# Optimization experiments

Hardware: AMD Instinct MI355X
Metric: run time of the kernel (lower is better)

The kernel has to match this reference:

```python
import jax, jax.numpy as jnp
import numpy as np

B, S, H, K = 64, 512, 1024, 7

def setup_inputs() -> dict:
    key = jax.random.key(0)
    ks = jax.random.split(key, 7)
    x = jax.random.normal(ks[0], (B, S, H), dtype=jnp.float32)
    gt = jax.random.randint(ks[1], (B, S), 0, K, dtype=jnp.int64)
    mask = jnp.ones((B, S), dtype=bool)
    # learned parameters
    W = jax.random.normal(ks[2], (H, K), dtype=jnp.float32) * (1.0 / np.sqrt(H))
    b = jnp.zeros((K,), dtype=jnp.float32)
    start_trans = jax.random.uniform(ks[3], (K,), minval=-0.1, maxval=0.1)
    end_trans = jax.random.uniform(ks[4], (K,), minval=-0.1, maxval=0.1)
    trans = jax.random.uniform(ks[5], (K, K), minval=-0.1, maxval=0.1)
    return {"x": x, "gt": gt, "mask": mask, "W": W, "b": b,
            "start_trans": start_trans, "end_trans": end_trans, "trans": trans}

def _crf_neg_llh(emissions, gt, mask, start_trans, end_trans, trans):
    # emissions: [B,S,K], gt: [B,S] int, mask: [B,S] bool
    maskf = mask.astype(emissions.dtype)
    # ---- numerator: score of gold path ----
    em_at_tag = jnp.take_along_axis(emissions, gt[..., None], axis=-1)[..., 0]  # [B,S]
    trans_sc = trans[gt[:, :-1], gt[:, 1:]]                                      # [B,S-1]
    num = start_trans[gt[:, 0]] + em_at_tag[:, 0]
    num = num + jnp.sum((trans_sc + em_at_tag[:, 1:]) * maskf[:, 1:], axis=1)
    last_idx = jnp.sum(mask, axis=1).astype(jnp.int32) - 1                       # [B]
    last_tags = jnp.take_along_axis(gt, last_idx[:, None], axis=1)[:, 0]
    num = num + end_trans[last_tags]
    # ---- denominator: log partition via forward algorithm (lax.scan) ----
    alpha0 = start_trans[None, :] + emissions[:, 0]                              # [B,K]
    em_rest = jnp.transpose(emissions[:, 1:], (1, 0, 2))                         # [S-1,B,K]
    m_rest = jnp.transpose(mask[:, 1:], (1, 0))                                  # [S-1,B]
    def step(alpha, inp):
        em_t, m_t = inp
        nxt = jax.nn.logsumexp(alpha[:, :, None] + trans[None, :, :] + em_t[:, None, :], axis=1)
        return jnp.where(m_t[:, None], nxt, alpha), None
    alpha, _ = jax.lax.scan(step, alpha0, (em_rest, m_rest))
    denom = jax.nn.logsumexp(alpha + end_trans[None, :], axis=1)                 # [B]
    llh = num - denom
    return -jnp.mean(llh)  # reduction='mean', module returns negative

def reference(x, gt, mask, W, b, start_trans, end_trans, trans):
    emissions = jnp.einsum('bsh,hk->bsk', x, W) + b
    return _crf_neg_llh(emissions, gt, mask, start_trans, end_trans, trans)
```

## Files before the change

### kernel.cpp

```cpp
#include <hip/hip_runtime.h>
#include <math.h>

#define NB 64
#define NS 512
#define NH 1024
#define NK 7
#define NCHUNK 16
#define CLEN 32

#define WPACK_F4 (14 * 512)

__global__ __launch_bounds__(256) void pack_w(const float* __restrict__ W,
                                              float4* __restrict__ Wpack)
{
    const int idx = blockIdx.x * 256 + threadIdx.x;
    if (idx >= WPACK_F4) return;
    const int j    = idx >> 9;
    const int t    = idx & 511;
    const int lane = t & 63;
    const int half = (t >> 6) & 1;
    const int cc   = j / NK;
    const int k    = j - cc * NK;
    const int hbase = half * 512 + (cc * 64 + lane) * 4;
    float4 v;
    v.x = W[(hbase + 0) * NK + k];
    v.y = W[(hbase + 1) * NK + k];
    v.z = W[(hbase + 2) * NK + k];
    v.w = W[(hbase + 3) * NK + k];
    Wpack[idx] = v;
}

__global__ __launch_bounds__(512, 4) void fused_emis_chunk(
    const float* __restrict__ x, const float4* __restrict__ Wpack,
    const float* __restrict__ bias, const float* __restrict__ trans,
    float* __restrict__ em, float* __restrict__ chunkP)
{
    __shared__ float lds_half[CLEN][2][8];
    __shared__ float lds_em[CLEN * 8];
    __shared__ float lds_tr[49];

    const int tid  = threadIdx.x;
    const int lane = tid & 63;
    const int wave = tid >> 6;
    const int pair = wave >> 1;
    const int half = wave & 1;
    const int b = blockIdx.x >> 4;
    const int c = blockIdx.x & (NCHUNK - 1);
    const int t0 = c * CLEN;
    const int row0 = b * NS + t0;

    if (tid < 49) lds_tr[tid] = trans[tid];

    float4 w4[2][NK];
#pragma unroll
    for (int cc = 0; cc < 2; ++cc)
#pragma unroll
        for (int k = 0; k < NK; ++k)
            w4[cc][k] = Wpack[(cc * NK + k) * 512 + tid];

    const float4* xbase = (const float4*)(x + (size_t)row0 * NH) + half * 128 + lane;

#pragma unroll 2
    for (int s = 0; s < 8; ++s) {
        const int r = pair + 4 * s;
        const float4* xr = xbase + (size_t)r * (NH / 4);
        const float4 v0 = xr[0];
        const float4 v1 = xr[64];
        float acc[NK];
#pragma unroll
        for (int k = 0; k < NK; ++k)
            acc[k] = v0.x * w4[0][k].x + v0.y * w4[0][k].y
                   + v0.z * w4[0][k].z + v0.w * w4[0][k].w
                   + v1.x * w4[1][k].x + v1.y * w4[1][k].y
                   + v1.z * w4[1][k].z + v1.w * w4[1][k].w;
#pragma unroll
        for (int m = 1; m < 8; m <<= 1)
#pragma unroll
            for (int k = 0; k < NK; ++k)
                acc[k] += __shfl_xor(acc[k], m, 64);
        const int ss = lane & 7;
        const float v01 = (ss & 1) ? acc[1] : acc[0];
        const float v23 = (ss & 1) ? acc[3] : acc[2];
        const float v45 = (ss & 1) ? acc[5] : acc[4];
        const float w03 = (ss & 2) ? v23 : v01;
        const float w47 = (ss & 2) ? acc[6] : v45;
        float v = (ss & 4) ? w47 : w03;
        v += __shfl_xor(v, 8, 64);
        v += __shfl_xor(v, 16, 64);
        v += __shfl_xor(v, 32, 64);
        if (lane < NK) lds_half[r][half][lane] = v;
    }
    __syncthreads();

    if (tid < CLEN * NK) {
        const int r = tid / NK;
        const int k = tid - r * NK;
        const float e = lds_half[r][0][k] + lds_half[r][1][k] + bias[k];
        lds_em[r * 8 + k] = e;
        em[(size_t)row0 * NK + tid] = e;
    }
    __syncthreads();
    if (wave != 0) return;

    const int li = lane < 49 ? lane : 48;
    const int i = li / 7;
    const int k = li - i * 7;
    float tj[NK];
#pragma unroll
    for (int j = 0; j < NK; ++j) tj[j] = lds_tr[j * 7 + k];

    const int first = (c == 0) ? 1 : 0;
    float P = lds_tr[i * 7 + k] + lds_em[first * 8 + k];
    for (int t = first + 1; t < CLEN; ++t) {
        float a[NK];
#pragma unroll
        for (int j = 0; j < NK; ++j)
            a[j] = __shfl(P, i * 7 + j, 64) + tj[j];
        const float m = fmaxf(fmaxf(fmaxf(a[0], a[1]), fmaxf(a[2], a[3])),
                              fmaxf(fmaxf(a[4], a[5]), a[6]));
        const float su = __expf(a[0]-m) + __expf(a[1]-m) + __expf(a[2]-m)
                       + __expf(a[3]-m) + __expf(a[4]-m) + __expf(a[5]-m)
                       + __expf(a[6]-m);
        P = m + __logf(su) + lds_em[t * 8 + k];
    }
    if (lane < 49)
        chunkP[(size_t)(b * NCHUNK + c) * 49 + lane] = P;
}

__global__ __launch_bounds__(64) void combine_kernel(
    const float* __restrict__ em, const float* __restrict__ chunkP,
    const int* __restrict__ gt32,
    const float* __restrict__ start_trans, const float* __restrict__ end_trans,
    const float* __restrict__ trans, float* __restrict__ out)
{
    __shared__ float lds_C[NCHUNK * 49];
    __shared__ float lds_tr[49];
    __shared__ int   lds_gt[NS];
    const int b    = blockIdx.x;
    const int lane = threadIdx.x;

    int oddbits = 0;
    for (int i = lane; i < 256; i += 64) oddbits |= gt32[2 * i + 1];
    const bool is64 = (__ballot(oddbits != 0) == 0ull);

    for (int idx = lane; idx < NCHUNK * 49; idx += 64)
        lds_C[idx] = chunkP[(size_t)b * NCHUNK * 49 + idx];
    for (int i = lane; i < NS; i += 64) {
        const int gidx = b * NS + i;
        lds_gt[i] = is64 ? gt32[2 * gidx] : gt32[gidx];
    }
    if (lane < 49) lds_tr[lane] = trans[lane];
    __syncthreads();

    const float* emb = em + (size_t)b * NS * NK;
    float numpart = 0.f;
#pragma unroll
    for (int ii = 0; ii < NS / 64; ++ii) {
        const int t = lane + 64 * ii;
        const int g = lds_gt[t];
        if (t == 0) numpart += start_trans[g] + emb[g];
        else        numpart += lds_tr[lds_gt[t - 1] * 7 + g] + emb[t * NK + g];
    }
#pragma unroll
    for (int m = 1; m < 64; m <<= 1) numpart += __shfl_xor(numpart, m, 64);
    const float num = numpart + end_trans[lds_gt[NS - 1]];

    const int kk = lane < NK ? lane : NK - 1;
    float alpha = start_trans[kk] + emb[kk];
#pragma unroll
    for (int c = 0; c < NCHUNK; ++c) {
        float a[NK];
#pragma unroll
        for (int j = 0; j < NK; ++j)
            a[j] = __shfl(alpha, j, 64) + lds_C[c * 49 + j * 7 + kk];
        const float m = fmaxf(fmaxf(fmaxf(a[0], a[1]), fmaxf(a[2], a[3])),
                              fmaxf(fmaxf(a[4], a[5]), a[6]));
        const float su = __expf(a[0]-m) + __expf(a[1]-m) + __expf(a[2]-m)
                       + __expf(a[3]-m) + __expf(a[4]-m) + __expf(a[5]-m)
                       + __expf(a[6]-m);
        alpha = m + __logf(su);
    }

    float v = (lane < NK) ? (alpha + end_trans[kk]) : -3.0e38f;
    float mv = v;
#pragma unroll
    for (int m = 1; m < 8; m <<= 1) mv = fmaxf(mv, __shfl_xor(mv, m, 64));
    float e = (lane < NK) ? __expf(v - mv) : 0.f;
#pragma unroll
    for (int m = 1; m < 8; m <<= 1) e += __shfl_xor(e, m, 64);
    if (lane == 0)
        atomicAdd(out, ((mv + __logf(e)) - num) * (1.0f / NB));
}

extern "C" void kernel_launch(void* const* d_in, const int* in_sizes, int n_in,
                              void* d_out, int out_size, void* d_ws, size_t ws_size,
                              hipStream_t stream)
{
    const float* x    = (const float*)d_in[0];
    const int*   gt   = (const int*)d_in[1];
    const float* W    = (const float*)d_in[3];
    const float* bias = (const float*)d_in[4];
    const float* st   = (const float*)d_in[5];
    const float* et   = (const float*)d_in[6];
    const float* tr   = (const float*)d_in[7];

    float4* Wpack = (float4*)d_ws;
    float*  em     = (float*)d_ws + (size_t)WPACK_F4 * 4;
    float*  chunkP = em + (size_t)NB * NS * NK;

    hipMemsetAsync(d_out, 0, sizeof(float) * out_size, stream);
    pack_w<<<(WPACK_F4 + 255) / 256, 256, 0, stream>>>(W, Wpack);
    fused_emis_chunk<<<NB * NCHUNK, 512, 0, stream>>>(x, Wpack, bias, tr, em, chunkP);
    combine_kernel<<<NB, 64, 0, stream>>>(em, chunkP, gt, st, et, tr, (float*)d_out);
}
```

Baseline: 232.0 us.

## Fuse weight packing, chunk scan, and combine into one kernel with atomic tickets

Merges the three kernels (W packing, emission+chunk scan, combine) into a single launch. Each block now transposes W into LDS itself, computes its chunk's gold-path numerator piece, and the last block per batch row (found via an atomic counter) runs the combine; a second counter elects a final block that writes the mean. This removes two kernel launches, the emission array write/read and the output memset. In exchange every block redoes the W transpose from global memory and the tail relies on threadfence-plus-counter ordering.

```diff
diff --git a/kernel.cpp b/kernel.cpp
--- a/kernel.cpp
+++ b/kernel.cpp
@@ -8,36 +8,29 @@
 #define NCHUNK 16
 #define CLEN 32
 
-#define WPACK_F4 (14 * 512)
-
-__global__ __launch_bounds__(256) void pack_w(const float* __restrict__ W,
-                                              float4* __restrict__ Wpack)
+#define WS_CNT     0
+#define WS_ALPHA0  80
+#define WS_NUMP    (WS_ALPHA0 + 64 * 8)
+#define WS_CHUNKP  (WS_NUMP + 64 * 16)
+#define WS_LLH     (WS_CHUNKP + 64 * 16 * 49)
+
+__global__ __launch_bounds__(512, 4) void crf_mega(
+    const float* __restrict__ x, const float* __restrict__ W,
+    const float* __restrict__ bias, const float* __restrict__ trans,
+    const float* __restrict__ start_trans, const float* __restrict__ end_trans,
+    const int* __restrict__ gt32,
+    int* __restrict__ cnt, float* __restrict__ ws, float* __restrict__ out)
 {
-    const int idx = blockIdx.x * 256 + threadIdx.x;
-    if (idx >= WPACK_F4) return;
-    const int j    = idx >> 9;
-    const int t    = idx & 511;
-    const int lane = t & 63;
-    const int half = (t >> 6) & 1;
-    const int cc   = j / NK;
-    const int k    = j - cc * NK;
-    const int hbase = half * 512 + (cc * 64 + lane) * 4;
-    float4 v;
-    v.x = W[(hbase + 0) * NK + k];
-    v.y = W[(hbase + 1) * NK + k];
-    v.z = W[(hbase + 2) * NK + k];
-    v.w = W[(hbase + 3) * NK + k];
-    Wpack[idx] = v;
-}
-
-__global__ __launch_bounds__(512, 4) void fused_emis_chunk(
-    const float* __restrict__ x, const float4* __restrict__ Wpack,
-    const float* __restrict__ bias, const float* __restrict__ trans,
-    float* __restrict__ em, float* __restrict__ chunkP)
-{
+    __shared__ float4 lds_w4[14 * 128];
     __shared__ float lds_half[CLEN][2][8];
     __shared__ float lds_em[CLEN * 8];
     __shared__ float lds_tr[49];
+    __shared__ float lds_C[NCHUNK * 49];
+
+    float* __restrict__ alpha0g = ws + WS_ALPHA0;
+    float* __restrict__ numP    = ws + WS_NUMP;
+    float* __restrict__ chunkP  = ws + WS_CHUNKP;
+    float* __restrict__ llh     = ws + WS_LLH;
 
     const int tid  = threadIdx.x;
     const int lane = tid & 63;
@@ -51,12 +44,29 @@
 
     if (tid < 49) lds_tr[tid] = trans[tid];
 
+    {
+        float* lds_wf = (float*)lds_w4;
+#pragma unroll
+        for (int q = 0; q < 14; ++q) {
+            const int e = tid + 512 * q;
+            const float val = W[e];
+            const int h  = e / 7;
+            const int k  = e - h * 7;
+            const int hw = h >> 9;
+            const int cw = (h >> 8) & 1;
+            const int lw = (h >> 2) & 63;
+            const int ii = h & 3;
+            lds_wf[(((cw * 7 + k) * 2 + hw) * 64 + lw) * 4 + ii] = val;
+        }
+    }
+    __syncthreads();
+
     float4 w4[2][NK];
 #pragma unroll
     for (int cc = 0; cc < 2; ++cc)
 #pragma unroll
         for (int k = 0; k < NK; ++k)
-            w4[cc][k] = Wpack[(cc * NK + k) * 512 + tid];
+            w4[cc][k] = lds_w4[(cc * NK + k) * 128 + half * 64 + lane];
 
     const float4* xbase = (const float4*)(x + (size_t)row0 * NH) + half * 128 + lane;
 
@@ -95,84 +105,89 @@
     if (tid < CLEN * NK) {
         const int r = tid / NK;
         const int k = tid - r * NK;
-        const float e = lds_half[r][0][k] + lds_half[r][1][k] + bias[k];
-        lds_em[r * 8 + k] = e;
-        em[(size_t)row0 * NK + tid] = e;
+        lds_em[r * 8 + k] = lds_half[r][0][k] + lds_half[r][1][k] + bias[k];
     }
     __syncthreads();
     if (wave != 0) return;
 
-    const int li = lane < 49 ? lane : 48;
-    const int i = li / 7;
-    const int k = li - i * 7;
-    float tj[NK];
-#pragma unroll
-    for (int j = 0; j < NK; ++j) tj[j] = lds_tr[j * 7 + k];
-
-    const int first = (c == 0) ? 1 : 0;
-    float P = lds_tr[i * 7 + k] + lds_em[first * 8 + k];
-    for (int t = first + 1; t < CLEN; ++t) {
-        float a[NK];
-#pragma unroll
-        for (int j = 0; j < NK; ++j)
-            a[j] = __shfl(P, i * 7 + j, 64) + tj[j];
-        const float m = fmaxf(fmaxf(fmaxf(a[0], a[1]), fmaxf(a[2], a[3])),
-                              fmaxf(fmaxf(a[4], a[5]), a[6]));
-        const float su = __expf(a[0]-m) + __expf(a[1]-m) + __expf(a[2]-m)
-                       + __expf(a[3]-m) + __expf(a[4]-m) + __expf(a[5]-m)
-                       + __expf(a[6]-m);
-        P = m + __logf(su) + lds_em[t * 8 + k];
-    }
-    if (lane < 49)
-        chunkP[(size_t)(b * NCHUNK + c) * 49 + lane] = P;
-}
-
-__global__ __launch_bounds__(64) void combine_kernel(
-    const float* __restrict__ em, const float* __restrict__ chunkP,
-    const int* __restrict__ gt32,
-    const float* __restrict__ start_trans, const float* __restrict__ end_trans,
-    const float* __restrict__ trans, float* __restrict__ out)
-{
-    __shared__ float lds_C[NCHUNK * 49];
-    __shared__ float lds_tr[49];
-    __shared__ int   lds_gt[NS];
-    const int b    = blockIdx.x;
-    const int lane = threadIdx.x;
 
     int oddbits = 0;
     for (int i = lane; i < 256; i += 64) oddbits |= gt32[2 * i + 1];
     const bool is64 = (__ballot(oddbits != 0) == 0ull);
 
+    {
+        const int tloc = lane & 31;
+        const int tg = t0 + tloc;
+        const int gidx = b * NS + tg;
+        const int g = is64 ? gt32[2 * gidx] : gt32[gidx];
+        float term = 0.f;
+        if (lane < 32) {
+            if (tg == 0) {
+                term = start_trans[g] + lds_em[g];
+            } else {
+                const int pidx = gidx - 1;
+                const int gp = is64 ? gt32[2 * pidx] : gt32[pidx];
+                term = lds_tr[gp * 7 + g] + lds_em[tloc * 8 + g];
+            }
+            if (tg == NS - 1) term += end_trans[g];
+        }
+#pragma unroll
+        for (int m = 1; m < 64; m <<= 1) term += __shfl_xor(term, m, 64);
+        if (lane == 0) numP[b * NCHUNK + c] = term;
+    }
+
+    if (c == 0 && lane < NK)
+        alpha0g[b * 8 + lane] = start_trans[lane] + lds_em[lane];
+
+    {
+        const int li = lane < 49 ? lane : 48;
+        const int i = li / 7;
+        const int k = li - i * 7;
+        float tj[NK];
+#pragma unroll
+        for (int j = 0; j < NK; ++j) tj[j] = lds_tr[j * 7 + k];
+
+        const int first = (c == 0) ? 1 : 0;
+        float P = lds_tr[i * 7 + k] + lds_em[first * 8 + k];
+        for (int t = first + 1; t < CLEN; ++t) {
+            float a[NK];
+#pragma unroll
+            for (int j = 0; j < NK; ++j)
+                a[j] = __shfl(P, i * 7 + j, 64) + tj[j];
+            const float m = fmaxf(fmaxf(fmaxf(a[0], a[1]), fmaxf(a[2], a[3])),
+                                  fmaxf(fmaxf(a[4], a[5]), a[6]));
+            const float su = __expf(a[0]-m) + __expf(a[1]-m) + __expf(a[2]-m)
+                           + __expf(a[3]-m) + __expf(a[4]-m) + __expf(a[5]-m)
+                           + __expf(a[6]-m);
+            P = m + __logf(su) + lds_em[t * 8 + k];
+        }
+        if (lane < 49)
+            chunkP[(size_t)(b * NCHUNK + c) * 49 + lane] = P;
+    }
+
+    __threadfence();
+    int old = 0;
+    if (lane == 0) old = atomicAdd(&cnt[b], 1);
+    old = __shfl(old, 0, 64);
+    if (old != NCHUNK - 1) return;
+    __threadfence();
+
     for (int idx = lane; idx < NCHUNK * 49; idx += 64)
         lds_C[idx] = chunkP[(size_t)b * NCHUNK * 49 + idx];
-    for (int i = lane; i < NS; i += 64) {
-        const int gidx = b * NS + i;
-        lds_gt[i] = is64 ? gt32[2 * gidx] : gt32[gidx];
-    }
-    if (lane < 49) lds_tr[lane] = trans[lane];
-    __syncthreads();
-
-    const float* emb = em + (size_t)b * NS * NK;
-    float numpart = 0.f;
-#pragma unroll
-    for (int ii = 0; ii < NS / 64; ++ii) {
-        const int t = lane + 64 * ii;
-        const int g = lds_gt[t];
-        if (t == 0) numpart += start_trans[g] + emb[g];
-        else        numpart += lds_tr[lds_gt[t - 1] * 7 + g] + emb[t * NK + g];
-    }
-#pragma unroll
-    for (int m = 1; m < 64; m <<= 1) numpart += __shfl_xor(numpart, m, 64);
-    const float num = numpart + end_trans[lds_gt[NS - 1]];
+
+    float np = (lane < NCHUNK) ? numP[b * NCHUNK + lane] : 0.f;
+#pragma unroll
+    for (int m = 1; m < 16; m <<= 1) np += __shfl_xor(np, m, 64);
+    const float num = __shfl(np, 0, 64);
 
     const int kk = lane < NK ? lane : NK - 1;
-    float alpha = start_trans[kk] + emb[kk];
-#pragma unroll
-    for (int c = 0; c < NCHUNK; ++c) {
+    float alpha = alpha0g[b * 8 + kk];
+#pragma unroll
+    for (int cc = 0; cc < NCHUNK; ++cc) {
         float a[NK];
 #pragma unroll
         for (int j = 0; j < NK; ++j)
-            a[j] = __shfl(alpha, j, 64) + lds_C[c * 49 + j * 7 + kk];
+            a[j] = __shfl(alpha, j, 64) + lds_C[cc * 49 + j * 7 + kk];
         const float m = fmaxf(fmaxf(fmaxf(a[0], a[1]), fmaxf(a[2], a[3])),
                               fmaxf(fmaxf(a[4], a[5]), a[6]));
         const float su = __expf(a[0]-m) + __expf(a[1]-m) + __expf(a[2]-m)
@@ -188,8 +203,19 @@
     float e = (lane < NK) ? __expf(v - mv) : 0.f;
 #pragma unroll
     for (int m = 1; m < 8; m <<= 1) e += __shfl_xor(e, m, 64);
-    if (lane == 0)
-        atomicAdd(out, ((mv + __logf(e)) - num) * (1.0f / NB));
+    if (lane == 0) llh[b] = (mv + __logf(e)) - num;
+
+    __threadfence();
+    int old2 = 0;
+    if (lane == 0) old2 = atomicAdd(&cnt[NB], 1);
+    old2 = __shfl(old2, 0, 64);
+    if (old2 != NB - 1) return;
+    __threadfence();
+
+    float s = llh[lane];
+#pragma unroll
+    for (int m = 1; m < 64; m <<= 1) s += __shfl_xor(s, m, 64);
+    if (lane == 0) out[0] = s * (1.0f / NB);
 }
 
 extern "C" void kernel_launch(void* const* d_in, const int* in_sizes, int n_in,
@@ -204,12 +230,10 @@
     const float* et   = (const float*)d_in[6];
     const float* tr   = (const float*)d_in[7];
 
-    float4* Wpack = (float4*)d_ws;
-    float*  em     = (float*)d_ws + (size_t)WPACK_F4 * 4;
-    float*  chunkP = em + (size_t)NB * NS * NK;
-
-    hipMemsetAsync(d_out, 0, sizeof(float) * out_size, stream);
-    pack_w<<<(WPACK_F4 + 255) / 256, 256, 0, stream>>>(W, Wpack);
-    fused_emis_chunk<<<NB * NCHUNK, 512, 0, stream>>>(x, Wpack, bias, tr, em, chunkP);
-    combine_kernel<<<NB, 64, 0, stream>>>(em, chunkP, gt, st, et, tr, (float*)d_out);
+    int*   cnt = (int*)d_ws;
+    float* ws  = (float*)d_ws;
+
+    hipMemsetAsync(cnt, 0, 80 * sizeof(int), stream);
+    crf_mega<<<NB * NCHUNK, 512, 0, stream>>>(x, W, bias, tr, st, et, gt,
+                                              cnt, ws, (float*)d_out);
 }
```

Result: slower. 271.9 us (+17.2%).
